# Performance work log

Measured on AMD Instinct MI355X. Metric: run time of the kernel, lower is better.

## Reference

```python
import jax, jax.numpy as jnp
import numpy as np

T, P, E, H = 200000, 100000, 600000, 256

def setup_inputs() -> dict:
    key = jax.random.key(0)
    ks = jax.random.split(key, 8)
    x = jax.random.normal(ks[0], (T, H), dtype=jnp.float32)
    points = jax.random.normal(ks[1], (P, 3), dtype=jnp.float32)
    triangles = jax.random.randint(ks[2], (T, 3), 0, P)
    triangle_edges = jax.random.randint(ks[3], (2, E), 0, T)
    din = H + 9
    W1 = jax.random.normal(ks[4], (din, H), dtype=jnp.float32) / np.sqrt(din)
    b1 = jnp.zeros((H,), dtype=jnp.float32)
    W2 = jax.random.normal(ks[5], (H, H), dtype=jnp.float32) / np.sqrt(H)
    b2 = jnp.zeros((H,), dtype=jnp.float32)
    return {"x": x, "points": points, "triangles": triangles,
            "triangle_edges": triangle_edges, "W1": W1, "b1": b1, "W2": W2, "b2": b2}

def reference(x, points, triangles, triangle_edges, W1, b1, W2, b2):
    # Per-triangle geometry: [T, 3(corners), 3(xyz)]
    tp = points[triangles]
    e_ij = tp[:, 0] - tp[:, 1]
    e_ik = tp[:, 0] - tp[:, 2]
    e_jk = tp[:, 1] - tp[:, 2]
    edge_vectors = jnp.stack([e_ij, e_ik, e_jk], axis=1)  # [T,3,3]
    t_max = jnp.max(edge_vectors, axis=1).astype(x.dtype)  # [T,3]
    t_min = jnp.min(edge_vectors, axis=1).astype(x.dtype)  # [T,3]
    barycenters = jnp.mean(tp, axis=1).astype(x.dtype)     # [T,3]

    src = triangle_edges[0]
    tgt = triangle_edges[1]
    # Relative geometric descriptor per edge: [E, 9]
    r_n_k = jnp.concatenate([t_min[src] - t_min[tgt],
                             t_max[src] - t_max[tgt],
                             barycenters[src] - barycenters[tgt]], axis=1)
    feature_diff = x[src] - x[tgt]                          # [E, H]
    mlp_in = jnp.concatenate([r_n_k, feature_diff], axis=1)  # [E, H+9]
    h = jax.nn.relu(mlp_in @ W1 + b1)
    mlp_out = h @ W2 + b2                                   # [E, H]
    # Scatter-add back to source triangles (order-independent sum)
    new_features = jax.ops.segment_sum(mlp_out, src, num_segments=x.shape[0])
    return new_features.astype(x.dtype)
```

## Files before the change

kernel.cpp:

```cpp
#include <hip/hip_runtime.h>
#include <stdint.h>

typedef float f32x4v __attribute__((ext_vector_type(4)));
typedef short short8v __attribute__((ext_vector_type(8)));

__device__ __forceinline__ float bf2f(unsigned short u) {
  union { uint32_t i; float f; } v; v.i = ((uint32_t)u) << 16; return v.f;
}
__device__ __forceinline__ unsigned short f2bf(float f) {
  union { float f; uint32_t i; } v; v.f = f;
  uint32_t x = v.i;
  uint32_t r = (x + 0x7FFFu + ((x >> 16) & 1u)) >> 16;
  return (unsigned short)r;
}

__global__ void prep_weights(const float* __restrict__ W1, const float* __restrict__ W2,
                             unsigned short* __restrict__ W1fT, unsigned short* __restrict__ W2T) {
  int i = blockIdx.x * blockDim.x + threadIdx.x;
  if (i < 256 * 288) {
    int n = i / 288, k = i % 288;
    float v = 0.f;
    if (k < 256) v = W1[(9 + k) * 256 + n];
    else if (k < 265) v = W1[(k - 256) * 256 + n];
    W1fT[i] = f2bf(v);
  }
  if (i < 256 * 256) {
    int n = i >> 8, k = i & 255;
    W2T[i] = f2bf(W2[k * 256 + n]);
  }
}

__global__ void geo_kernel(const float* __restrict__ points, const int* __restrict__ tri,
                           float* __restrict__ geo12, int T) {
  int t = blockIdx.x * blockDim.x + threadIdx.x;
  if (t >= T) return;
  int i0 = tri[3 * t], i1 = tri[3 * t + 1], i2 = tri[3 * t + 2];
  float g[12];
#pragma unroll
  for (int c = 0; c < 3; ++c) {
    float p0 = points[i0 * 3 + c], p1 = points[i1 * 3 + c], p2 = points[i2 * 3 + c];
    float e0 = p0 - p1, e1 = p0 - p2, e2 = p1 - p2;
    float mx = fmaxf(e0, fmaxf(e1, e2));
    float mn = fminf(e0, fminf(e1, e2));
    float bc = (p0 + p1 + p2) * (1.0f / 3.0f);
    g[c] = mn; g[3 + c] = mx; g[6 + c] = bc;
  }
  g[9] = 0.f; g[10] = 0.f; g[11] = 0.f;
  float4* o = (float4*)(geo12 + (size_t)t * 12);
  o[0] = make_float4(g[0], g[1], g[2], g[3]);
  o[1] = make_float4(g[4], g[5], g[6], g[7]);
  o[2] = make_float4(g[8], g[9], g[10], g[11]);
}

__global__ void count_kernel(const int* __restrict__ te, int* __restrict__ count, int E) {
  int e = blockIdx.x * blockDim.x + threadIdx.x;
  if (e < E) atomicAdd(&count[te[e]], 1);
}

__global__ void scan1_kernel(const int* __restrict__ count, int* __restrict__ incl,
                             int* __restrict__ blocksum, int T) {
  __shared__ int wsums[4];
  int tid = threadIdx.x, wave = tid >> 6, lane = tid & 63;
  int idx0 = blockIdx.x * 1024 + tid * 4;
  int c0 = 0, c1 = 0, c2 = 0, c3 = 0;
  if (idx0 + 3 < T) {
    int4 v = *(const int4*)(count + idx0);
    c0 = v.x; c1 = v.y; c2 = v.z; c3 = v.w;
  } else {
    if (idx0 < T) c0 = count[idx0];
    if (idx0 + 1 < T) c1 = count[idx0 + 1];
    if (idx0 + 2 < T) c2 = count[idx0 + 2];
  }
  int s = c0 + c1 + c2 + c3;
  int inclv = s;
#pragma unroll
  for (int off = 1; off < 64; off <<= 1) {
    int n = __shfl_up(inclv, off);
    if (lane >= off) inclv += n;
  }
  if (lane == 63) wsums[wave] = inclv;
  __syncthreads();
  int wbase = 0;
#pragma unroll
  for (int w = 0; w < 4; ++w) if (w < wave) wbase += wsums[w];
  int base = wbase + inclv - s;
  int e0 = base + c0, e1 = e0 + c1, e2 = e1 + c2, e3 = e2 + c3;
  if (idx0 < T) incl[idx0] = e0;
  if (idx0 + 1 < T) incl[idx0 + 1] = e1;
  if (idx0 + 2 < T) incl[idx0 + 2] = e2;
  if (idx0 + 3 < T) incl[idx0 + 3] = e3;
  if (tid == 255) blocksum[blockIdx.x] = wbase + inclv;
}

__global__ void scan2_kernel(const int* __restrict__ blocksum, int* __restrict__ blockbase, int nb) {
  __shared__ int wsums[4];
  int tid = threadIdx.x, wave = tid >> 6, lane = tid & 63;
  int v = (tid < nb) ? blocksum[tid] : 0;
  int inclv = v;
#pragma unroll
  for (int off = 1; off < 64; off <<= 1) {
    int n = __shfl_up(inclv, off);
    if (lane >= off) inclv += n;
  }
  if (lane == 63) wsums[wave] = inclv;
  __syncthreads();
  int wbase = 0;
#pragma unroll
  for (int w = 0; w < 4; ++w) if (w < wave) wbase += wsums[w];
  if (tid < nb) blockbase[tid] = wbase + inclv - v;
}

__global__ void scan3_kernel(const int* __restrict__ count, const int* __restrict__ incl,
                             const int* __restrict__ blockbase, int* __restrict__ offsets,
                             int* __restrict__ cursor, int T) {
  int idx = blockIdx.x * 1024 + threadIdx.x * 4;
  int bb = blockbase[blockIdx.x];
#pragma unroll
  for (int j = 0; j < 4; ++j) {
    int i = idx + j;
    if (i < T) {
      int o = incl[i] + bb;
      offsets[i + 1] = o;
      cursor[i] = o - count[i];
    }
  }
  if (blockIdx.x == 0 && threadIdx.x == 0) offsets[0] = 0;
}

__global__ void fill_kernel(const int* __restrict__ te, int* __restrict__ cursor,
                            int* __restrict__ tgt_list, int E) {
  int e = blockIdx.x * blockDim.x + threadIdx.x;
  if (e < E) {
    int s = te[e];
    int pos = atomicAdd(&cursor[s], 1);
    tgt_list[pos] = te[E + e];
  }
}

__launch_bounds__(256)
__global__ void ugemm_kernel(const float* __restrict__ x, const float* __restrict__ geo12,
                             const unsigned short* __restrict__ W1fT,
                             unsigned short* __restrict__ U, int T) {
  __shared__ alignas(16) unsigned short Al[64][40];
  int m0 = blockIdx.x * 64;
  int tid = threadIdx.x;
  int wid = tid >> 6, lane = tid & 63;
  int srow = tid >> 2, cq = tid & 3;
  int l15 = lane & 15, lhi = lane >> 4;
  int nbase = wid * 64;
  f32x4v acc[4][4] = {};
  const unsigned short* bp[4];
#pragma unroll
  for (int nf = 0; nf < 4; ++nf)
    bp[nf] = W1fT + (size_t)(nbase + nf * 16 + l15) * 288 + 8 * lhi;
  for (int kk = 0; kk < 9; ++kk) {
    int k0 = kk * 32;
    int t = m0 + srow;
    float f[8];
    if (kk < 8) {
      const float* sp = x + (size_t)t * 256 + k0 + cq * 8;
      float4 a = (t < T) ? *(const float4*)sp : make_float4(0, 0, 0, 0);
      float4 b = (t < T) ? *(const float4*)(sp + 4) : make_float4(0, 0, 0, 0);
      f[0] = a.x; f[1] = a.y; f[2] = a.z; f[3] = a.w;
      f[4] = b.x; f[5] = b.y; f[6] = b.z; f[7] = b.w;
    } else {
      if (cq == 0 && t < T) {
        float4 a = *(const float4*)(geo12 + (size_t)t * 12);
        float4 b = *(const float4*)(geo12 + (size_t)t * 12 + 4);
        f[0] = a.x; f[1] = a.y; f[2] = a.z; f[3] = a.w;
        f[4] = b.x; f[5] = b.y; f[6] = b.z; f[7] = b.w;
      } else if (cq == 1 && t < T) {
        float4 a = *(const float4*)(geo12 + (size_t)t * 12 + 8);
        f[0] = a.x; f[1] = a.y; f[2] = a.z; f[3] = a.w;
        f[4] = 0.f; f[5] = 0.f; f[6] = 0.f; f[7] = 0.f;
      } else {
        f[0] = f[1] = f[2] = f[3] = f[4] = f[5] = f[6] = f[7] = 0.f;
      }
    }
    short8v av;
#pragma unroll
    for (int j = 0; j < 8; ++j) av[j] = (short)f2bf(f[j]);
    *(short8v*)(&Al[srow][cq * 8]) = av;
    __syncthreads();
    short8v a[4];
#pragma unroll
    for (int mi = 0; mi < 4; ++mi)
      a[mi] = *(const short8v*)(&Al[mi * 16 + l15][8 * lhi]);
#pragma unroll
    for (int nf = 0; nf < 4; ++nf) {
      short8v b = *(const short8v*)(bp[nf] + k0);
#pragma unroll
      for (int mi = 0; mi < 4; ++mi)
        acc[mi][nf] = __builtin_amdgcn_mfma_f32_16x16x32_bf16(a[mi], b, acc[mi][nf], 0, 0, 0);
    }
    __syncthreads();
  }
#pragma unroll
  for (int mi = 0; mi < 4; ++mi) {
#pragma unroll
    for (int i = 0; i < 4; ++i) {
      int m = m0 + mi * 16 + 4 * lhi + i;
      if (m < T) {
#pragma unroll
        for (int nf = 0; nf < 4; ++nf) {
          int n = nbase + nf * 16 + l15;
          U[(size_t)m * 256 + n] = f2bf(acc[mi][nf][i]);
        }
      }
    }
  }
}

__launch_bounds__(256)
__global__ void fused_kernel(const unsigned short* __restrict__ U,
                             const unsigned short* __restrict__ W2T,
                             const int* __restrict__ offsets,
                             const int* __restrict__ count,
                             const int* __restrict__ tgt_list,
                             const float* __restrict__ b1,
                             const float* __restrict__ b2,
                             float* __restrict__ out, int T) {
  __shared__ alignas(16) unsigned short hl[32][264];
  int t0 = blockIdx.x * 32;
  int tid = threadIdx.x, wid = tid >> 6, lane = tid & 63;
  int c8 = (tid & 31) * 8;
  float b1r[8];
  {
    float4 a = *(const float4*)(b1 + c8);
    float4 b = *(const float4*)(b1 + c8 + 4);
    b1r[0] = a.x; b1r[1] = a.y; b1r[2] = a.z; b1r[3] = a.w;
    b1r[4] = b.x; b1r[5] = b.y; b1r[6] = b.z; b1r[7] = b.w;
  }
#pragma unroll 1
  for (int b = 0; b < 4; ++b) {
    int r = b * 8 + (tid >> 5);
    int t = t0 + r;
    int beg = offsets[t], end = offsets[t + 1];
    short8v uvv = *(const short8v*)(U + (size_t)t * 256 + c8);
    float u[8], s[8];
#pragma unroll
    for (int j = 0; j < 8; ++j) { u[j] = bf2f((unsigned short)uvv[j]); s[j] = 0.f; }
    for (int ei = beg; ei < end; ei += 4) {
      int last = end - 1;
      int i1 = (ei + 1 <= last) ? ei + 1 : last;
      int i2 = (ei + 2 <= last) ? ei + 2 : last;
      int i3 = (ei + 3 <= last) ? ei + 3 : last;
      int g0 = tgt_list[ei], g1 = tgt_list[i1], g2 = tgt_list[i2], g3 = tgt_list[i3];
      short8v v0 = *(const short8v*)(U + (size_t)g0 * 256 + c8);
      short8v v1 = *(const short8v*)(U + (size_t)g1 * 256 + c8);
      short8v v2 = *(const short8v*)(U + (size_t)g2 * 256 + c8);
      short8v v3 = *(const short8v*)(U + (size_t)g3 * 256 + c8);
      float m1 = (ei + 1 <= last) ? 1.f : 0.f;
      float m2 = (ei + 2 <= last) ? 1.f : 0.f;
      float m3 = (ei + 3 <= last) ? 1.f : 0.f;
#pragma unroll
      for (int j = 0; j < 8; ++j) {
        float ub = u[j] + b1r[j];
        s[j] += fmaxf(ub - bf2f((unsigned short)v0[j]), 0.f)
              + m1 * fmaxf(ub - bf2f((unsigned short)v1[j]), 0.f)
              + m2 * fmaxf(ub - bf2f((unsigned short)v2[j]), 0.f)
              + m3 * fmaxf(ub - bf2f((unsigned short)v3[j]), 0.f);
      }
    }
    short8v hv;
#pragma unroll
    for (int j = 0; j < 8; ++j) hv[j] = (short)f2bf(s[j]);
    *(short8v*)(&hl[r][c8]) = hv;
  }
  __syncthreads();
  f32x4v acc[2][4] = {};
  int l15 = lane & 15, lhi = lane >> 4;
  int nbase = wid * 64;
  const unsigned short* bp[4];
  float b2r[4];
#pragma unroll
  for (int nf = 0; nf < 4; ++nf) {
    bp[nf] = W2T + (size_t)(nbase + nf * 16 + l15) * 256 + 8 * lhi;
    b2r[nf] = b2[nbase + nf * 16 + l15];
  }
  for (int kk = 0; kk < 8; ++kk) {
    int k0 = kk * 32;
    short8v a0 = *(const short8v*)(&hl[l15][k0 + 8 * lhi]);
    short8v a1 = *(const short8v*)(&hl[16 + l15][k0 + 8 * lhi]);
#pragma unroll
    for (int nf = 0; nf < 4; ++nf) {
      short8v bv = *(const short8v*)(bp[nf] + k0);
      acc[0][nf] = __builtin_amdgcn_mfma_f32_16x16x32_bf16(a0, bv, acc[0][nf], 0, 0, 0);
      acc[1][nf] = __builtin_amdgcn_mfma_f32_16x16x32_bf16(a1, bv, acc[1][nf], 0, 0, 0);
    }
  }
#pragma unroll
  for (int mi = 0; mi < 2; ++mi) {
#pragma unroll
    for (int i = 0; i < 4; ++i) {
      int m = mi * 16 + 4 * lhi + i;
      int t = t0 + m;
      if (t < T) {
        float cnt = (float)count[t];
#pragma unroll
        for (int nf = 0; nf < 4; ++nf) {
          int n = nbase + nf * 16 + l15;
          out[(size_t)t * 256 + n] = acc[mi][nf][i] + cnt * b2r[nf];
        }
      }
    }
  }
}

extern "C" void kernel_launch(void* const* d_in, const int* in_sizes, int n_in,
                              void* d_out, int out_size, void* d_ws, size_t ws_size,
                              hipStream_t stream) {
  const float* x = (const float*)d_in[0];
  const float* points = (const float*)d_in[1];
  const int* triangles = (const int*)d_in[2];
  const int* te = (const int*)d_in[3];
  const float* W1 = (const float*)d_in[4];
  const float* b1 = (const float*)d_in[5];
  const float* W2 = (const float*)d_in[6];
  const float* b2 = (const float*)d_in[7];
  float* out = (float*)d_out;
  int T = in_sizes[0] / 256;
  int E = in_sizes[3] / 2;

  char* ws = (char*)d_ws;
  size_t off = 0;
  auto alloc = [&](size_t bytes) {
    void* p = ws + off;
    off = (off + bytes + 255) & ~(size_t)255;
    return p;
  };
  unsigned short* U     = (unsigned short*)alloc((size_t)T * 256 * 2);
  float*          geo12 = (float*)alloc((size_t)T * 12 * 4);
  unsigned short* W1fT  = (unsigned short*)alloc((size_t)256 * 288 * 2);
  unsigned short* W2T   = (unsigned short*)alloc((size_t)256 * 256 * 2);
  int* count   = (int*)alloc((size_t)T * 4);
  int* offsets = (int*)alloc((size_t)(T + 1) * 4);
  int* cursor  = (int*)alloc((size_t)T * 4);
  int* tgtl    = (int*)alloc((size_t)E * 4);
  int* incl    = (int*)alloc((size_t)T * 4);
  int* bsum    = (int*)alloc(256 * 4);
  int* bbase   = (int*)alloc(256 * 4);
  if (off > ws_size) return;

  int nb1 = (T + 1023) / 1024;
  hipMemsetAsync(count, 0, (size_t)T * 4, stream);
  prep_weights<<<288, 256, 0, stream>>>(W1, W2, W1fT, W2T);
  geo_kernel<<<(T + 255) / 256, 256, 0, stream>>>(points, triangles, geo12, T);
  count_kernel<<<(E + 255) / 256, 256, 0, stream>>>(te, count, E);
  scan1_kernel<<<nb1, 256, 0, stream>>>(count, incl, bsum, T);
  scan2_kernel<<<1, 256, 0, stream>>>(bsum, bbase, nb1);
  scan3_kernel<<<nb1, 256, 0, stream>>>(count, incl, bbase, offsets, cursor, T);
  fill_kernel<<<(E + 255) / 256, 256, 0, stream>>>(te, cursor, tgtl, E);
  ugemm_kernel<<<(T + 63) / 64, 256, 0, stream>>>(x, geo12, W1fT, U, T);
  fused_kernel<<<(T + 31) / 32, 256, 0, stream>>>(U, W2T, offsets, count, tgtl, b1, b2, out, T);
}
```

Baseline: 361.7 us.

## Double-buffer ugemm LDS tiles and widen fused kernel to 1024 threads

The U-GEMM kernel now double-buffers its shared A tile, prefetching the next K-slice from global memory while the MFMAs on the current slice run, and it drops the per-row bounds checks. The fused gather/second-GEMM kernel launches 1024 threads per block so each thread handles one triangle row instead of looping over four. Its W2 GEMM is split across 16 waves, and b1 is folded into u once. This aims to hide load latency and raise parallelism in the gather phase. It relies on T being a multiple of 64 and 32, since the bounds checks are gone.

```diff
diff --git a/kernel.cpp b/kernel.cpp
--- a/kernel.cpp
+++ b/kernel.cpp
@@ -141,7 +141,7 @@
 __global__ void ugemm_kernel(const float* __restrict__ x, const float* __restrict__ geo12,
                              const unsigned short* __restrict__ W1fT,
                              unsigned short* __restrict__ U, int T) {
-  __shared__ alignas(16) unsigned short Al[64][40];
+  __shared__ alignas(16) unsigned short Al[2][64][40];
   int m0 = blockIdx.x * 64;
   int tid = threadIdx.x;
   int wid = tid >> 6, lane = tid & 63;
@@ -153,23 +153,22 @@
 #pragma unroll
   for (int nf = 0; nf < 4; ++nf)
     bp[nf] = W1fT + (size_t)(nbase + nf * 16 + l15) * 288 + 8 * lhi;
-  for (int kk = 0; kk < 9; ++kk) {
-    int k0 = kk * 32;
-    int t = m0 + srow;
-    float f[8];
+  int t = m0 + srow;
+
+  auto loadf = [&](int kk, float* f) {
     if (kk < 8) {
-      const float* sp = x + (size_t)t * 256 + k0 + cq * 8;
-      float4 a = (t < T) ? *(const float4*)sp : make_float4(0, 0, 0, 0);
-      float4 b = (t < T) ? *(const float4*)(sp + 4) : make_float4(0, 0, 0, 0);
+      const float* sp = x + (size_t)t * 256 + kk * 32 + cq * 8;
+      float4 a = *(const float4*)sp;
+      float4 b = *(const float4*)(sp + 4);
       f[0] = a.x; f[1] = a.y; f[2] = a.z; f[3] = a.w;
       f[4] = b.x; f[5] = b.y; f[6] = b.z; f[7] = b.w;
     } else {
-      if (cq == 0 && t < T) {
+      if (cq == 0) {
         float4 a = *(const float4*)(geo12 + (size_t)t * 12);
         float4 b = *(const float4*)(geo12 + (size_t)t * 12 + 4);
         f[0] = a.x; f[1] = a.y; f[2] = a.z; f[3] = a.w;
         f[4] = b.x; f[5] = b.y; f[6] = b.z; f[7] = b.w;
-      } else if (cq == 1 && t < T) {
+      } else if (cq == 1) {
         float4 a = *(const float4*)(geo12 + (size_t)t * 12 + 8);
         f[0] = a.x; f[1] = a.y; f[2] = a.z; f[3] = a.w;
         f[4] = 0.f; f[5] = 0.f; f[6] = 0.f; f[7] = 0.f;
@@ -177,22 +176,39 @@
         f[0] = f[1] = f[2] = f[3] = f[4] = f[5] = f[6] = f[7] = 0.f;
       }
     }
+  };
+
+  {
+    float f[8];
+    loadf(0, f);
     short8v av;
 #pragma unroll
     for (int j = 0; j < 8; ++j) av[j] = (short)f2bf(f[j]);
-    *(short8v*)(&Al[srow][cq * 8]) = av;
-    __syncthreads();
+    *(short8v*)(&Al[0][srow][cq * 8]) = av;
+  }
+  __syncthreads();
+
+  for (int kk = 0; kk < 9; ++kk) {
+    int cur = kk & 1;
+    float fn[8];
+    if (kk < 8) loadf(kk + 1, fn);
     short8v a[4];
 #pragma unroll
     for (int mi = 0; mi < 4; ++mi)
-      a[mi] = *(const short8v*)(&Al[mi * 16 + l15][8 * lhi]);
+      a[mi] = *(const short8v*)(&Al[cur][mi * 16 + l15][8 * lhi]);
 #pragma unroll
     for (int nf = 0; nf < 4; ++nf) {
-      short8v b = *(const short8v*)(bp[nf] + k0);
+      short8v b = *(const short8v*)(bp[nf] + kk * 32);
 #pragma unroll
       for (int mi = 0; mi < 4; ++mi)
         acc[mi][nf] = __builtin_amdgcn_mfma_f32_16x16x32_bf16(a[mi], b, acc[mi][nf], 0, 0, 0);
     }
+    if (kk < 8) {
+      short8v av;
+#pragma unroll
+      for (int j = 0; j < 8; ++j) av[j] = (short)f2bf(fn[j]);
+      *(short8v*)(&Al[cur ^ 1][srow][cq * 8]) = av;
+    }
     __syncthreads();
   }
 #pragma unroll
@@ -200,18 +216,16 @@
 #pragma unroll
     for (int i = 0; i < 4; ++i) {
       int m = m0 + mi * 16 + 4 * lhi + i;
-      if (m < T) {
-#pragma unroll
-        for (int nf = 0; nf < 4; ++nf) {
-          int n = nbase + nf * 16 + l15;
-          U[(size_t)m * 256 + n] = f2bf(acc[mi][nf][i]);
-        }
+#pragma unroll
+      for (int nf = 0; nf < 4; ++nf) {
+        int n = nbase + nf * 16 + l15;
+        U[(size_t)m * 256 + n] = f2bf(acc[mi][nf][i]);
       }
     }
   }
 }
 
-__launch_bounds__(256)
+__launch_bounds__(1024, 8)
 __global__ void fused_kernel(const unsigned short* __restrict__ U,
                              const unsigned short* __restrict__ W2T,
                              const int* __restrict__ offsets,
@@ -222,24 +236,23 @@
                              float* __restrict__ out, int T) {
   __shared__ alignas(16) unsigned short hl[32][264];
   int t0 = blockIdx.x * 32;
-  int tid = threadIdx.x, wid = tid >> 6, lane = tid & 63;
+  int tid = threadIdx.x;
+  int row = tid >> 5;
   int c8 = (tid & 31) * 8;
-  float b1r[8];
   {
-    float4 a = *(const float4*)(b1 + c8);
-    float4 b = *(const float4*)(b1 + c8 + 4);
-    b1r[0] = a.x; b1r[1] = a.y; b1r[2] = a.z; b1r[3] = a.w;
-    b1r[4] = b.x; b1r[5] = b.y; b1r[6] = b.z; b1r[7] = b.w;
-  }
-#pragma unroll 1
-  for (int b = 0; b < 4; ++b) {
-    int r = b * 8 + (tid >> 5);
-    int t = t0 + r;
+    int t = t0 + row;
     int beg = offsets[t], end = offsets[t + 1];
+    float b1r[8];
+    {
+      float4 a = *(const float4*)(b1 + c8);
+      float4 b = *(const float4*)(b1 + c8 + 4);
+      b1r[0] = a.x; b1r[1] = a.y; b1r[2] = a.z; b1r[3] = a.w;
+      b1r[4] = b.x; b1r[5] = b.y; b1r[6] = b.z; b1r[7] = b.w;
+    }
     short8v uvv = *(const short8v*)(U + (size_t)t * 256 + c8);
     float u[8], s[8];
 #pragma unroll
-    for (int j = 0; j < 8; ++j) { u[j] = bf2f((unsigned short)uvv[j]); s[j] = 0.f; }
+    for (int j = 0; j < 8; ++j) { u[j] = bf2f((unsigned short)uvv[j]) + b1r[j]; s[j] = 0.f; }
     for (int ei = beg; ei < end; ei += 4) {
       int last = end - 1;
       int i1 = (ei + 1 <= last) ? ei + 1 : last;
@@ -255,54 +268,46 @@
       float m3 = (ei + 3 <= last) ? 1.f : 0.f;
 #pragma unroll
       for (int j = 0; j < 8; ++j) {
-        float ub = u[j] + b1r[j];
-        s[j] += fmaxf(ub - bf2f((unsigned short)v0[j]), 0.f)
-              + m1 * fmaxf(ub - bf2f((unsigned short)v1[j]), 0.f)
-              + m2 * fmaxf(ub - bf2f((unsigned short)v2[j]), 0.f)
-              + m3 * fmaxf(ub - bf2f((unsigned short)v3[j]), 0.f);
+        s[j] += fmaxf(u[j] - bf2f((unsigned short)v0[j]), 0.f)
+              + m1 * fmaxf(u[j] - bf2f((unsigned short)v1[j]), 0.f)
+              + m2 * fmaxf(u[j] - bf2f((unsigned short)v2[j]), 0.f)
+              + m3 * fmaxf(u[j] - bf2f((unsigned short)v3[j]), 0.f);
       }
     }
     short8v hv;
 #pragma unroll
     for (int j = 0; j < 8; ++j) hv[j] = (short)f2bf(s[j]);
-    *(short8v*)(&hl[r][c8]) = hv;
+    *(short8v*)(&hl[row][c8]) = hv;
   }
   __syncthreads();
-  f32x4v acc[2][4] = {};
+  int wid = tid >> 6, lane = tid & 63;
   int l15 = lane & 15, lhi = lane >> 4;
-  int nbase = wid * 64;
-  const unsigned short* bp[4];
-  float b2r[4];
-#pragma unroll
-  for (int nf = 0; nf < 4; ++nf) {
-    bp[nf] = W2T + (size_t)(nbase + nf * 16 + l15) * 256 + 8 * lhi;
-    b2r[nf] = b2[nbase + nf * 16 + l15];
+  int mh = wid >> 3, ns = wid & 7;
+  f32x4v acc[2] = {};
+  const unsigned short* bp[2];
+  float b2r[2];
+#pragma unroll
+  for (int nf = 0; nf < 2; ++nf) {
+    bp[nf] = W2T + (size_t)(ns * 32 + nf * 16 + l15) * 256 + 8 * lhi;
+    b2r[nf] = b2[ns * 32 + nf * 16 + l15];
   }
   for (int kk = 0; kk < 8; ++kk) {
     int k0 = kk * 32;
-    short8v a0 = *(const short8v*)(&hl[l15][k0 + 8 * lhi]);
-    short8v a1 = *(const short8v*)(&hl[16 + l15][k0 + 8 * lhi]);
-#pragma unroll
-    for (int nf = 0; nf < 4; ++nf) {
+    short8v a = *(const short8v*)(&hl[mh * 16 + l15][k0 + 8 * lhi]);
+#pragma unroll
+    for (int nf = 0; nf < 2; ++nf) {
       short8v bv = *(const short8v*)(bp[nf] + k0);
-      acc[0][nf] = __builtin_amdgcn_mfma_f32_16x16x32_bf16(a0, bv, acc[0][nf], 0, 0, 0);
-      acc[1][nf] = __builtin_amdgcn_mfma_f32_16x16x32_bf16(a1, bv, acc[1][nf], 0, 0, 0);
-    }
-  }
-#pragma unroll
-  for (int mi = 0; mi < 2; ++mi) {
-#pragma unroll
-    for (int i = 0; i < 4; ++i) {
-      int m = mi * 16 + 4 * lhi + i;
-      int t = t0 + m;
-      if (t < T) {
-        float cnt = (float)count[t];
-#pragma unroll
-        for (int nf = 0; nf < 4; ++nf) {
-          int n = nbase + nf * 16 + l15;
-          out[(size_t)t * 256 + n] = acc[mi][nf][i] + cnt * b2r[nf];
-        }
-      }
+      acc[nf] = __builtin_amdgcn_mfma_f32_16x16x32_bf16(a, bv, acc[nf], 0, 0, 0);
+    }
+  }
+#pragma unroll
+  for (int i = 0; i < 4; ++i) {
+    int t = t0 + mh * 16 + 4 * lhi + i;
+    float cnt = (float)count[t];
+#pragma unroll
+    for (int nf = 0; nf < 2; ++nf) {
+      int n = ns * 32 + nf * 16 + l15;
+      out[(size_t)t * 256 + n] = acc[nf][i] + cnt * b2r[nf];
     }
   }
 }
@@ -352,5 +357,5 @@
   scan3_kernel<<<nb1, 256, 0, stream>>>(count, incl, bbase, offsets, cursor, T);
   fill_kernel<<<(E + 255) / 256, 256, 0, stream>>>(te, cursor, tgtl, E);
   ugemm_kernel<<<(T + 63) / 64, 256, 0, stream>>>(x, geo12, W1fT, U, T);
-  fused_kernel<<<(T + 31) / 32, 256, 0, stream>>>(U, W2T, offsets, count, tgtl, b1, b2, out, T);
-}
+  fused_kernel<<<(T + 31) / 32, 1024, 0, stream>>>(U, W2T, offsets, count, tgtl, b1, b2, out, T);
+}
```

New measurement: 448.4 us. 24.0% more time.
